# Optimization experiments

Measured on AMD Instinct MI355X. Metric: run time of the kernel, lower is better.

The kernel has to match this reference:

```python
import jax, jax.numpy as jnp
import numpy as np


def setup_inputs() -> dict:
    key = jax.random.key(0)
    k1, k2, k3 = jax.random.split(key, 3)
    vol_shape = (4, 1, 128, 192, 192)   # [B, C, D, H, W]
    dsc_shape = (4, 1, 8, 12, 12)       # PatchGAN-style discriminator logits
    return {
        "dsc_fake": jax.random.normal(k1, dsc_shape, dtype=jnp.float32),
        "predicts": jax.random.normal(k2, vol_shape, dtype=jnp.float32),
        "y_data": jax.random.normal(k3, vol_shape, dtype=jnp.float32),
        "zeros": jnp.zeros(dsc_shape, dtype=jnp.float32),
    }


def reference(dsc_fake, predicts, y_data, zeros):
    # BCE with logits (stable form), target = zeros
    bce = jnp.mean(
        jnp.maximum(dsc_fake, 0.0) - dsc_fake * zeros
        + jnp.log1p(jnp.exp(-jnp.abs(dsc_fake)))
    )
    # L1 loss between target volume and prediction
    g_loss_l1 = jnp.mean(jnp.abs(y_data - predicts))
    # Finite-difference gradient MSE along D, H, W (axes 2,3,4).
    # Original detaches to numpy, so this term carries no gradient.
    yd = jax.lax.stop_gradient(y_data)
    pr = jax.lax.stop_gradient(predicts)
    g_loss_gd = jnp.float32(0.0)
    for ax in (2, 3, 4):
        gy = jnp.abs(jnp.gradient(yd, axis=ax))   # central diff interior, one-sided edges
        gp = jnp.abs(jnp.gradient(pr, axis=ax))
        g_loss_gd = g_loss_gd + jnp.mean((gy - gp) ** 2)
    return bce + 100.0 * g_loss_l1 + 100.0 * g_loss_gd
```

## Files before the change

kernel.cpp:

```cpp
#include <hip/hip_runtime.h>
#include <math.h>

namespace {
constexpr int BATCH = 4;
constexpr int DDIM  = 128;
constexpr int HDIM  = 192;
constexpr int WDIM  = 192;
constexpr long long NTOT = (long long)BATCH * DDIM * HDIM * WDIM;
constexpr int NDSC  = 4 * 1 * 8 * 12 * 12;

constexpr int DT     = 8;
constexpr int NDC    = DDIM / DT;
constexpr int HB     = 16;
constexpr int NHB    = HDIM / HB;
constexpr int BLOCKV = 256;
constexpr int GRIDV  = BATCH * NDC * NHB;
constexpr int PLSTR  = HDIM * WDIM;
constexpr int BLOCKF = 256;
}

#define GTERM(dy, dp, s2) { float t0_ = fabsf(dy) - fabsf(dp); gd = fmaf(t0_ * t0_, (s2), gd); }

__device__ __forceinline__ float4 shup16(float4 v) {
    float4 r;
    r.x = __shfl_up(v.x, 16, 64); r.y = __shfl_up(v.y, 16, 64);
    r.z = __shfl_up(v.z, 16, 64); r.w = __shfl_up(v.w, 16, 64);
    return r;
}
__device__ __forceinline__ float4 shdn16(float4 v) {
    float4 r;
    r.x = __shfl_down(v.x, 16, 64); r.y = __shfl_down(v.y, 16, 64);
    r.z = __shfl_down(v.z, 16, 64); r.w = __shfl_down(v.w, 16, 64);
    return r;
}
__device__ __forceinline__ float4 sel4(bool c, float4 a, float4 b) {
    float4 r;
    r.x = c ? a.x : b.x; r.y = c ? a.y : b.y;
    r.z = c ? a.z : b.z; r.w = c ? a.w : b.w;
    return r;
}

__global__ __launch_bounds__(BLOCKV, 2) void vol_kernel(const float* __restrict__ p,
                                                        const float* __restrict__ y,
                                                        const float* __restrict__ dsc,
                                                        float* __restrict__ part) {
    const int tid  = threadIdx.x;
    const int wv   = tid >> 6;
    const int lane = tid & 63;
    const int r    = lane >> 4;
    const int i16  = lane & 15;
    const int w0   = i16 * 12;

    const int blk0 = blockIdx.x;
    const int swz  = (blk0 & 7) * (GRIDV / 8) + (blk0 >> 3);
    const int hb   = swz % NHB;
    const int rest = swz / NHB;
    const int dc   = rest % NDC;
    const int b    = rest / NDC;
    const int h0w  = hb * HB + wv * 4;
    const int h    = h0w + r;
    const int d0   = dc * DT;
    const int rb   = (r < 2) ? (h0w > 0 ? h0w - 1 : 0)
                             : (h0w + 4 < HDIM ? h0w + 4 : HDIM - 1);

    const long long base = (long long)(b * DDIM) * PLSTR;
    const float* yO = y + base + h  * WDIM + w0;
    const float* pO = p + base + h  * WDIM + w0;
    const float* yB = y + base + rb * WDIM + w0;
    const float* pB = p + base + rb * WDIM + w0;

    float4 ymY[3], ymP[3], ycY[3], ycP[3], cnY[3], cnP[3];
    {
        const int pm = d0 ? d0 - 1 : 0;
        #pragma unroll
        for (int g = 0; g < 3; ++g) {
            ymY[g] = *(const float4*)(yO + pm * PLSTR + 4 * g);
            ymP[g] = *(const float4*)(pO + pm * PLSTR + 4 * g);
            ycY[g] = *(const float4*)(yO + d0 * PLSTR + 4 * g);
            ycP[g] = *(const float4*)(pO + d0 * PLSTR + 4 * g);
            cnY[g] = *(const float4*)(yO + (d0 + 1) * PLSTR + 4 * g);
            cnP[g] = *(const float4*)(pO + (d0 + 1) * PLSTR + 4 * g);
        }
    }

    float l1 = 0.f, gd = 0.f;
    const float s2h  = (h == 0 || h == HDIM - 1) ? 1.f : 0.25f;
    const float s2w0 = (i16 == 0)  ? 1.f : 0.25f;
    const float s2w3 = (i16 == 15) ? 1.f : 0.25f;

    #pragma unroll 1
    for (int i = 0; i < DT; ++i) {
        const int e = d0 + i;

        const int p2 = (e + 2 < DDIM) ? e + 2 : DDIM - 1;
        float4 nuY[3], nuP[3], bmY[3], bmP[3];
        #pragma unroll
        for (int g = 0; g < 3; ++g) {
            nuY[g] = *(const float4*)(yO + p2 * PLSTR + 4 * g);
            nuP[g] = *(const float4*)(pO + p2 * PLSTR + 4 * g);
            bmY[g] = *(const float4*)(yB + e  * PLSTR + 4 * g);
            bmP[g] = *(const float4*)(pB + e  * PLSTR + 4 * g);
        }

        const float s2d = (e == 0 || e == DDIM - 1) ? 1.f : 0.25f;

        float wlY = __shfl_up (ycY[2].w, 1, 64);
        float wrY = __shfl_down(ycY[0].x, 1, 64);
        float wlP = __shfl_up (ycP[2].w, 1, 64);
        float wrP = __shfl_down(ycP[0].x, 1, 64);
        wlY = (i16 == 0)  ? ycY[0].x : wlY;  wlP = (i16 == 0)  ? ycP[0].x : wlP;
        wrY = (i16 == 15) ? ycY[2].w : wrY;  wrP = (i16 == 15) ? ycP[2].w : wrP;

        #pragma unroll
        for (int g = 0; g < 3; ++g) {
            const float4 ay = ycY[g], ap = ycP[g];
            const float4 my = ymY[g], mp = ymP[g];
            const float4 ny = cnY[g], np2 = cnP[g];

            l1 += fabsf(ay.x - ap.x) + fabsf(ay.y - ap.y)
                + fabsf(ay.z - ap.z) + fabsf(ay.w - ap.w);

            const float4 hmy = sel4(r == 0, bmY[g], shup16(ay));
            const float4 hmp = sel4(r == 0, bmP[g], shup16(ap));
            const float4 hpy = sel4(r == 3, bmY[g], shdn16(ay));
            const float4 hpp = sel4(r == 3, bmP[g], shdn16(ap));
            GTERM(hpy.x - hmy.x, hpp.x - hmp.x, s2h);
            GTERM(hpy.y - hmy.y, hpp.y - hmp.y, s2h);
            GTERM(hpy.z - hmy.z, hpp.z - hmp.z, s2h);
            GTERM(hpy.w - hmy.w, hpp.w - hmp.w, s2h);

            GTERM(ny.x - my.x, np2.x - mp.x, s2d);
            GTERM(ny.y - my.y, np2.y - mp.y, s2d);
            GTERM(ny.z - my.z, np2.z - mp.z, s2d);
            GTERM(ny.w - my.w, np2.w - mp.w, s2d);
        }
        {
            const float4 a0 = ycY[0], a1 = ycY[1], a2 = ycY[2];
            const float4 p0 = ycP[0], p1 = ycP[1], p2v = ycP[2];
            GTERM(a0.y - wlY , p0.y - wlP , s2w0);
            GTERM(a0.z - a0.x, p0.z - p0.x, 0.25f);
            GTERM(a0.w - a0.y, p0.w - p0.y, 0.25f);
            GTERM(a1.x - a0.z, p1.x - p0.z, 0.25f);
            GTERM(a1.y - a0.w, p1.y - p0.w, 0.25f);
            GTERM(a1.z - a1.x, p1.z - p1.x, 0.25f);
            GTERM(a1.w - a1.y, p1.w - p1.y, 0.25f);
            GTERM(a2.x - a1.z, p2v.x - p1.z, 0.25f);
            GTERM(a2.y - a1.w, p2v.y - p1.w, 0.25f);
            GTERM(a2.z - a2.x, p2v.z - p2v.x, 0.25f);
            GTERM(a2.w - a2.y, p2v.w - p2v.y, 0.25f);
            GTERM(wrY  - a2.z, wrP  - p2v.z, s2w3);
        }

        #pragma unroll
        for (int g = 0; g < 3; ++g) {
            ymY[g] = ycY[g]; ymP[g] = ycP[g];
            ycY[g] = cnY[g]; ycP[g] = cnP[g];
            cnY[g] = nuY[g]; cnP[g] = nuP[g];
        }
    }

    float s = 0.f;
    {
        const int gi = blk0 * BLOCKV + tid;
        if (gi < NDSC) {
            const float x = dsc[gi];
            s = fmaxf(x, 0.f) + log1pf(expf(-fabsf(x)));
        }
    }

    __shared__ float red1[4], red2[4], red3[4];
    #pragma unroll
    for (int off = 32; off > 0; off >>= 1) {
        l1 += __shfl_down(l1, off, 64);
        gd += __shfl_down(gd, off, 64);
        s  += __shfl_down(s,  off, 64);
    }
    if (lane == 0) { red1[wv] = l1; red2[wv] = gd; red3[wv] = s; }
    __syncthreads();
    if (tid == 0) {
        part[3 * blk0]     = red1[0] + red1[1] + red1[2] + red1[3];
        part[3 * blk0 + 1] = red2[0] + red2[1] + red2[2] + red2[3];
        part[3 * blk0 + 2] = red3[0] + red3[1] + red3[2] + red3[3];
    }
}

__global__ __launch_bounds__(BLOCKF) void finalize_kernel(const float* __restrict__ part,
                                                          float* __restrict__ out) {
    float l1 = 0.f, gd = 0.f, s = 0.f;
    for (int i = threadIdx.x; i < GRIDV; i += BLOCKF) {
        l1 += part[3 * i];
        gd += part[3 * i + 1];
        s  += part[3 * i + 2];
    }
    __shared__ float a[4], c[4], e2[4];
    #pragma unroll
    for (int off = 32; off > 0; off >>= 1) {
        l1 += __shfl_down(l1, off, 64);
        gd += __shfl_down(gd, off, 64);
        s  += __shfl_down(s,  off, 64);
    }
    if ((threadIdx.x & 63) == 0) {
        const int w = threadIdx.x >> 6;
        a[w] = l1; c[w] = gd; e2[w] = s;
    }
    __syncthreads();
    if (threadIdx.x == 0) {
        const float bce = (e2[0] + e2[1] + e2[2] + e2[3]) / (float)NDSC;
        const float l1m = (a[0] + a[1] + a[2] + a[3]) / (float)NTOT;
        const float gdm = (c[0] + c[1] + c[2] + c[3]) / (float)NTOT;
        out[0] = bce + 100.f * (l1m + gdm);
    }
}

extern "C" void kernel_launch(void* const* d_in, const int* in_sizes, int n_in,
                              void* d_out, int out_size, void* d_ws, size_t ws_size,
                              hipStream_t stream) {
    const float* dsc_fake = (const float*)d_in[0];
    const float* predicts = (const float*)d_in[1];
    const float* y_data   = (const float*)d_in[2];
    float* part = (float*)d_ws;
    float* out  = (float*)d_out;

    vol_kernel<<<GRIDV, BLOCKV, 0, stream>>>(predicts, y_data, dsc_fake, part);
    finalize_kernel<<<1, BLOCKF, 0, stream>>>(part, out);
}
```

Measured before the change: 177.3 us.

## Replace D-marching register-reuse stencil with one-point-per-thread direct neighbor loads

Drops the per-block march along D, where each thread carried a 12-wide W strip and rotated register planes, in favour of a flat grid where each thread handles one 4-wide float4 at a single (b,d,h). All six stencil neighbours are loaded straight from global memory instead of being reused through registers and cross-lane shuffles. This raises the occupancy hint and grid size to expose more memory parallelism, and reduces register pressure. The cost is reading each element several times (relying on L2/cache for reuse) and producing many more partial sums for the finalize kernel, which is widened to 512 threads.

```diff
diff --git a/kernel.cpp b/kernel.cpp
--- a/kernel.cpp
+++ b/kernel.cpp
@@ -9,155 +9,81 @@
 constexpr long long NTOT = (long long)BATCH * DDIM * HDIM * WDIM;
 constexpr int NDSC  = 4 * 1 * 8 * 12 * 12;
 
-constexpr int DT     = 8;
-constexpr int NDC    = DDIM / DT;
-constexpr int HB     = 16;
-constexpr int NHB    = HDIM / HB;
 constexpr int BLOCKV = 256;
-constexpr int GRIDV  = BATCH * NDC * NHB;
+constexpr int WT     = 3;
+constexpr int HTIL   = 12;
+constexpr int GRIDV  = BATCH * DDIM * HTIL * WT;
 constexpr int PLSTR  = HDIM * WDIM;
-constexpr int BLOCKF = 256;
+constexpr int BLOCKF = 512;
 }
 
 #define GTERM(dy, dp, s2) { float t0_ = fabsf(dy) - fabsf(dp); gd = fmaf(t0_ * t0_, (s2), gd); }
 
-__device__ __forceinline__ float4 shup16(float4 v) {
-    float4 r;
-    r.x = __shfl_up(v.x, 16, 64); r.y = __shfl_up(v.y, 16, 64);
-    r.z = __shfl_up(v.z, 16, 64); r.w = __shfl_up(v.w, 16, 64);
-    return r;
-}
-__device__ __forceinline__ float4 shdn16(float4 v) {
-    float4 r;
-    r.x = __shfl_down(v.x, 16, 64); r.y = __shfl_down(v.y, 16, 64);
-    r.z = __shfl_down(v.z, 16, 64); r.w = __shfl_down(v.w, 16, 64);
-    return r;
-}
-__device__ __forceinline__ float4 sel4(bool c, float4 a, float4 b) {
-    float4 r;
-    r.x = c ? a.x : b.x; r.y = c ? a.y : b.y;
-    r.z = c ? a.z : b.z; r.w = c ? a.w : b.w;
-    return r;
-}
-
-__global__ __launch_bounds__(BLOCKV, 2) void vol_kernel(const float* __restrict__ p,
+__global__ __launch_bounds__(BLOCKV, 6) void vol_kernel(const float* __restrict__ p,
                                                         const float* __restrict__ y,
                                                         const float* __restrict__ dsc,
                                                         float* __restrict__ part) {
     const int tid  = threadIdx.x;
-    const int wv   = tid >> 6;
-    const int lane = tid & 63;
-    const int r    = lane >> 4;
-    const int i16  = lane & 15;
-    const int w0   = i16 * 12;
+    const int i16  = tid & 15;
+    const int r    = tid >> 4;
 
     const int blk0 = blockIdx.x;
     const int swz  = (blk0 & 7) * (GRIDV / 8) + (blk0 >> 3);
-    const int hb   = swz % NHB;
-    const int rest = swz / NHB;
-    const int dc   = rest % NDC;
-    const int b    = rest / NDC;
-    const int h0w  = hb * HB + wv * 4;
-    const int h    = h0w + r;
-    const int d0   = dc * DT;
-    const int rb   = (r < 2) ? (h0w > 0 ? h0w - 1 : 0)
-                             : (h0w + 4 < HDIM ? h0w + 4 : HDIM - 1);
+    const int d    = swz % DDIM;
+    int rest       = swz / DDIM;
+    const int wt   = rest % WT;  rest /= WT;
+    const int ht   = rest % HTIL;
+    const int b    = rest / HTIL;
+    const int h    = ht * 16 + r;
+    const int w0   = wt * 64 + i16 * 4;
 
-    const long long base = (long long)(b * DDIM) * PLSTR;
-    const float* yO = y + base + h  * WDIM + w0;
-    const float* pO = p + base + h  * WDIM + w0;
-    const float* yB = y + base + rb * WDIM + w0;
-    const float* pB = p + base + rb * WDIM + w0;
+    const int dm = d ? d - 1 : 0;
+    const int dp = (d < DDIM - 1) ? d + 1 : DDIM - 1;
+    const int hm = h ? h - 1 : 0;
+    const int hp = (h < HDIM - 1) ? h + 1 : HDIM - 1;
+    const int wl = w0 ? w0 - 1 : 0;
+    const int wr = (w0 + 4 < WDIM) ? w0 + 4 : WDIM - 1;
 
-    float4 ymY[3], ymP[3], ycY[3], ycP[3], cnY[3], cnP[3];
-    {
-        const int pm = d0 ? d0 - 1 : 0;
-        #pragma unroll
-        for (int g = 0; g < 3; ++g) {
-            ymY[g] = *(const float4*)(yO + pm * PLSTR + 4 * g);
-            ymP[g] = *(const float4*)(pO + pm * PLSTR + 4 * g);
-            ycY[g] = *(const float4*)(yO + d0 * PLSTR + 4 * g);
-            ycP[g] = *(const float4*)(pO + d0 * PLSTR + 4 * g);
-            cnY[g] = *(const float4*)(yO + (d0 + 1) * PLSTR + 4 * g);
-            cnP[g] = *(const float4*)(pO + (d0 + 1) * PLSTR + 4 * g);
-        }
-    }
+    const int bb  = b * DDIM;
+    const int ic  = ((bb + d ) * HDIM + h ) * WDIM;
+    const int ihm = ((bb + d ) * HDIM + hm) * WDIM + w0;
+    const int ihp = ((bb + d ) * HDIM + hp) * WDIM + w0;
+    const int idm = ((bb + dm) * HDIM + h ) * WDIM + w0;
+    const int idp = ((bb + dp) * HDIM + h ) * WDIM + w0;
 
-    float l1 = 0.f, gd = 0.f;
+    const float4 ycv = *(const float4*)(y + ic + w0);
+    const float4 pcv = *(const float4*)(p + ic + w0);
+    const float4 yhm = *(const float4*)(y + ihm);
+    const float4 yhp = *(const float4*)(y + ihp);
+    const float4 phm = *(const float4*)(p + ihm);
+    const float4 php = *(const float4*)(p + ihp);
+    const float4 ydm = *(const float4*)(y + idm);
+    const float4 ydp = *(const float4*)(y + idp);
+    const float4 pdm = *(const float4*)(p + idm);
+    const float4 pdp = *(const float4*)(p + idp);
+    const float  ywl = y[ic + wl], ywr = y[ic + wr];
+    const float  pwl = p[ic + wl], pwr = p[ic + wr];
+
     const float s2h  = (h == 0 || h == HDIM - 1) ? 1.f : 0.25f;
-    const float s2w0 = (i16 == 0)  ? 1.f : 0.25f;
-    const float s2w3 = (i16 == 15) ? 1.f : 0.25f;
+    const float s2d  = (d == 0 || d == DDIM - 1) ? 1.f : 0.25f;
+    const float s2w0 = (w0 == 0)            ? 1.f : 0.25f;
+    const float s2w3 = (w0 + 3 == WDIM - 1) ? 1.f : 0.25f;
 
-    #pragma unroll 1
-    for (int i = 0; i < DT; ++i) {
-        const int e = d0 + i;
-
-        const int p2 = (e + 2 < DDIM) ? e + 2 : DDIM - 1;
-        float4 nuY[3], nuP[3], bmY[3], bmP[3];
-        #pragma unroll
-        for (int g = 0; g < 3; ++g) {
-            nuY[g] = *(const float4*)(yO + p2 * PLSTR + 4 * g);
-            nuP[g] = *(const float4*)(pO + p2 * PLSTR + 4 * g);
-            bmY[g] = *(const float4*)(yB + e  * PLSTR + 4 * g);
-            bmP[g] = *(const float4*)(pB + e  * PLSTR + 4 * g);
-        }
-
-        const float s2d = (e == 0 || e == DDIM - 1) ? 1.f : 0.25f;
-
-        float wlY = __shfl_up (ycY[2].w, 1, 64);
-        float wrY = __shfl_down(ycY[0].x, 1, 64);
-        float wlP = __shfl_up (ycP[2].w, 1, 64);
-        float wrP = __shfl_down(ycP[0].x, 1, 64);
-        wlY = (i16 == 0)  ? ycY[0].x : wlY;  wlP = (i16 == 0)  ? ycP[0].x : wlP;
-        wrY = (i16 == 15) ? ycY[2].w : wrY;  wrP = (i16 == 15) ? ycP[2].w : wrP;
-
-        #pragma unroll
-        for (int g = 0; g < 3; ++g) {
-            const float4 ay = ycY[g], ap = ycP[g];
-            const float4 my = ymY[g], mp = ymP[g];
-            const float4 ny = cnY[g], np2 = cnP[g];
-
-            l1 += fabsf(ay.x - ap.x) + fabsf(ay.y - ap.y)
-                + fabsf(ay.z - ap.z) + fabsf(ay.w - ap.w);
-
-            const float4 hmy = sel4(r == 0, bmY[g], shup16(ay));
-            const float4 hmp = sel4(r == 0, bmP[g], shup16(ap));
-            const float4 hpy = sel4(r == 3, bmY[g], shdn16(ay));
-            const float4 hpp = sel4(r == 3, bmP[g], shdn16(ap));
-            GTERM(hpy.x - hmy.x, hpp.x - hmp.x, s2h);
-            GTERM(hpy.y - hmy.y, hpp.y - hmp.y, s2h);
-            GTERM(hpy.z - hmy.z, hpp.z - hmp.z, s2h);
-            GTERM(hpy.w - hmy.w, hpp.w - hmp.w, s2h);
-
-            GTERM(ny.x - my.x, np2.x - mp.x, s2d);
-            GTERM(ny.y - my.y, np2.y - mp.y, s2d);
-            GTERM(ny.z - my.z, np2.z - mp.z, s2d);
-            GTERM(ny.w - my.w, np2.w - mp.w, s2d);
-        }
-        {
-            const float4 a0 = ycY[0], a1 = ycY[1], a2 = ycY[2];
-            const float4 p0 = ycP[0], p1 = ycP[1], p2v = ycP[2];
-            GTERM(a0.y - wlY , p0.y - wlP , s2w0);
-            GTERM(a0.z - a0.x, p0.z - p0.x, 0.25f);
-            GTERM(a0.w - a0.y, p0.w - p0.y, 0.25f);
-            GTERM(a1.x - a0.z, p1.x - p0.z, 0.25f);
-            GTERM(a1.y - a0.w, p1.y - p0.w, 0.25f);
-            GTERM(a1.z - a1.x, p1.z - p1.x, 0.25f);
-            GTERM(a1.w - a1.y, p1.w - p1.y, 0.25f);
-            GTERM(a2.x - a1.z, p2v.x - p1.z, 0.25f);
-            GTERM(a2.y - a1.w, p2v.y - p1.w, 0.25f);
-            GTERM(a2.z - a2.x, p2v.z - p2v.x, 0.25f);
-            GTERM(a2.w - a2.y, p2v.w - p2v.y, 0.25f);
-            GTERM(wrY  - a2.z, wrP  - p2v.z, s2w3);
-        }
-
-        #pragma unroll
-        for (int g = 0; g < 3; ++g) {
-            ymY[g] = ycY[g]; ymP[g] = ycP[g];
-            ycY[g] = cnY[g]; ycP[g] = cnP[g];
-            cnY[g] = nuY[g]; cnP[g] = nuP[g];
-        }
-    }
+    float l1, gd = 0.f;
+    l1 = fabsf(ycv.x - pcv.x) + fabsf(ycv.y - pcv.y)
+       + fabsf(ycv.z - pcv.z) + fabsf(ycv.w - pcv.w);
+    GTERM(ycv.y - ywl  , pcv.y - pwl  , s2w0);
+    GTERM(ycv.z - ycv.x, pcv.z - pcv.x, 0.25f);
+    GTERM(ycv.w - ycv.y, pcv.w - pcv.y, 0.25f);
+    GTERM(ywr   - ycv.z, pwr   - pcv.z, s2w3);
+    GTERM(yhp.x - yhm.x, php.x - phm.x, s2h);
+    GTERM(yhp.y - yhm.y, php.y - phm.y, s2h);
+    GTERM(yhp.z - yhm.z, php.z - phm.z, s2h);
+    GTERM(yhp.w - yhm.w, php.w - phm.w, s2h);
+    GTERM(ydp.x - ydm.x, pdp.x - pdm.x, s2d);
+    GTERM(ydp.y - ydm.y, pdp.y - pdm.y, s2d);
+    GTERM(ydp.z - ydm.z, pdp.z - pdm.z, s2d);
+    GTERM(ydp.w - ydm.w, pdp.w - pdm.w, s2d);
 
     float s = 0.f;
     {
@@ -169,6 +95,8 @@
     }
 
     __shared__ float red1[4], red2[4], red3[4];
+    const int wv   = tid >> 6;
+    const int lane = tid & 63;
     #pragma unroll
     for (int off = 32; off > 0; off >>= 1) {
         l1 += __shfl_down(l1, off, 64);
@@ -192,7 +120,7 @@
         gd += part[3 * i + 1];
         s  += part[3 * i + 2];
     }
-    __shared__ float a[4], c[4], e2[4];
+    __shared__ float a[8], c[8], e2[8];
     #pragma unroll
     for (int off = 32; off > 0; off >>= 1) {
         l1 += __shfl_down(l1, off, 64);
@@ -205,9 +133,12 @@
     }
     __syncthreads();
     if (threadIdx.x == 0) {
-        const float bce = (e2[0] + e2[1] + e2[2] + e2[3]) / (float)NDSC;
-        const float l1m = (a[0] + a[1] + a[2] + a[3]) / (float)NTOT;
-        const float gdm = (c[0] + c[1] + c[2] + c[3]) / (float)NTOT;
+        float tl = 0.f, tg = 0.f, ts = 0.f;
+        #pragma unroll
+        for (int w = 0; w < BLOCKF / 64; ++w) { tl += a[w]; tg += c[w]; ts += e2[w]; }
+        const float bce = ts / (float)NDSC;
+        const float l1m = tl / (float)NTOT;
+        const float gdm = tg / (float)NTOT;
         out[0] = bce + 100.f * (l1m + gdm);
     }
 }
```

Result: slower. 205.7 us (+16.0%).
